# Performance work log

Measured on AMD Instinct MI355X. Metric: run time of the kernel, lower is better.

Reference implementation:

```python
import jax, jax.numpy as jnp
import numpy as np

VOCAB = 32000
EMB = 512
HEADS = 8
HEAD_DIM = EMB // HEADS
MLP = 2048
LAYERS = 6
KERNEL_EPS = 1e-3  # performer generalized-attention kernel_epsilon
LN_EPS = 1e-6


def sinusoidal_pos_emb(seq_len, dim):
    pos = np.arange(seq_len)[:, None].astype(np.float32)
    div = np.exp(np.arange(0, dim, 2).astype(np.float32) * (-np.log(10000.0) / dim))
    pe = np.zeros((seq_len, dim), dtype=np.float32)
    pe[:, 0::2] = np.sin(pos * div)
    pe[:, 1::2] = np.cos(pos * div)
    return jnp.asarray(pe)


def setup_inputs() -> dict:
    key = jax.random.key(0)
    ks = jax.random.split(key, 16)
    B, S = 4, 4096
    s_emb = 1.0 / np.sqrt(EMB)
    s_head = 1.0 / np.sqrt(HEAD_DIM)
    s_mlp = 1.0 / np.sqrt(MLP)
    return {
        'tokens': jax.random.randint(ks[0], (B, S), 0, VOCAB),
        'embed': jax.random.normal(ks[1], (VOCAB, EMB), jnp.float32) * s_emb,
        'Wq': jax.random.normal(ks[2], (LAYERS, EMB, HEADS, HEAD_DIM), jnp.float32) * s_emb,
        'Wk': jax.random.normal(ks[3], (LAYERS, EMB, HEADS, HEAD_DIM), jnp.float32) * s_emb,
        'Wv': jax.random.normal(ks[4], (LAYERS, EMB, HEADS, HEAD_DIM), jnp.float32) * s_emb,
        'Wo': jax.random.normal(ks[5], (LAYERS, HEADS, HEAD_DIM, EMB), jnp.float32) * s_head,
        'ln1_s': jnp.ones((LAYERS, EMB), jnp.float32),
        'ln1_b': jnp.zeros((LAYERS, EMB), jnp.float32),
        'W1': jax.random.normal(ks[6], (LAYERS, EMB, MLP), jnp.float32) * s_emb,
        'b1': jnp.zeros((LAYERS, MLP), jnp.float32),
        'W2': jax.random.normal(ks[7], (LAYERS, MLP, EMB), jnp.float32) * s_mlp,
        'b2': jnp.zeros((LAYERS, EMB), jnp.float32),
        'ln2_s': jnp.ones((LAYERS, EMB), jnp.float32),
        'ln2_b': jnp.zeros((LAYERS, EMB), jnp.float32),
        'lnf_s': jnp.ones((EMB,), jnp.float32),
        'lnf_b': jnp.zeros((EMB,), jnp.float32),
    }


def layer_norm(x, s, b):
    mu = jnp.mean(x, axis=-1, keepdims=True)
    var = jnp.mean(jnp.square(x - mu), axis=-1, keepdims=True)
    return (x - mu) * jax.lax.rsqrt(var + LN_EPS) * s + b


def favor_generalized_attention(x, Wq, Wk, Wv, Wo):
    # Performer generalized attention, deterministic ReLU feature map,
    # renormalized (bidirectional): O(S * m * d) linear attention.
    q = jnp.einsum('bsd,dhf->bshf', x, Wq)
    k = jnp.einsum('bsd,dhf->bshf', x, Wk)
    v = jnp.einsum('bsd,dhf->bshf', x, Wv)
    pq = jax.nn.relu(q) + KERNEL_EPS  # phi(q): [B,S,H,F]
    pk = jax.nn.relu(k) + KERNEL_EPS  # phi(k)
    kv = jnp.einsum('bshf,bshe->bhfe', pk, v)          # [B,H,F,E]
    num = jnp.einsum('bshf,bhfe->bshe', pq, kv)        # numerator
    den = jnp.einsum('bshf,bhf->bsh', pq, pk.sum(axis=1))  # renormalizer
    attn = num / den[..., None]
    return jnp.einsum('bshe,hed->bsd', attn, Wo)


def reference(tokens, embed, Wq, Wk, Wv, Wo, ln1_s, ln1_b, W1, b1, W2, b2,
              ln2_s, ln2_b, lnf_s, lnf_b):
    B, S = tokens.shape
    x = embed[tokens] + sinusoidal_pos_emb(S, EMB)[None, :, :]
    for l in range(LAYERS):
        h = layer_norm(x, ln1_s[l], ln1_b[l])
        x = x + favor_generalized_attention(h, Wq[l], Wk[l], Wv[l], Wo[l])
        h = layer_norm(x, ln2_s[l], ln2_b[l])
        h = jax.nn.gelu(h @ W1[l] + b1[l]) @ W2[l] + b2[l]
        x = x + h
    return layer_norm(x, lnf_s, lnf_b)
```

## Files before the change

### kernel.cpp

```cpp
#include <hip/hip_runtime.h>

typedef float f32x4 __attribute__((ext_vector_type(4)));
typedef __bf16 bf16x8 __attribute__((ext_vector_type(8)));

#define NROWS 16384
#define SEQ   4096
#define EMBD  512
#define MLPD  2048

__device__ inline float gelu_tanh(float x) {
    float t = 0.7978845608028654f * (x + 0.044715f * x * x * x);
    float e = __expf(2.f * t);
    float th = 1.f - 2.f / (1.f + e);
    return 0.5f * x * (1.f + th);
}

#define GLOAD16(gp, lp)                                                        \
    __builtin_amdgcn_global_load_lds(                                          \
        (const __attribute__((address_space(1))) void*)(gp),                   \
        (__attribute__((address_space(3))) void*)(lp), 16, 0, 0)

__global__ void pos_kernel(float* __restrict__ pos) {
    int i = blockIdx.x * 256 + threadIdx.x;
    int s = i >> 8, j = i & 255;
    float div = __expf((float)j * (-2.f * 9.210340371976184f / 512.f));
    float a = (float)s * div;
    pos[(size_t)s * 512 + 2 * j]     = sinf(a);
    pos[(size_t)s * 512 + 2 * j + 1] = cosf(a);
}

__global__ void embed_kernel(const int* __restrict__ tokens,
                             const float* __restrict__ embed,
                             const float* __restrict__ pos,
                             float* __restrict__ x) {
    int row = blockIdx.x;
    int t = threadIdx.x;
    int s = row & (SEQ - 1);
    int tok = tokens[row];
    f32x4 e = *(const f32x4*)(embed + (size_t)tok * 512 + t * 4);
    f32x4 p = *(const f32x4*)(pos + (size_t)s * 512 + t * 4);
    e += p;
    *(f32x4*)(x + (size_t)row * 512 + t * 4) = e;
}

__global__ void transpose_bf16(const float* __restrict__ in, __bf16* __restrict__ out,
                               int K, int N, size_t in_lstride, size_t out_lstride) {
    __shared__ float tile[32][33];
    in  += (size_t)blockIdx.z * in_lstride;
    out += (size_t)blockIdx.z * out_lstride;
    int n0 = blockIdx.x * 32, k0 = blockIdx.y * 32;
    int tx = threadIdx.x, ty = threadIdx.y;
    #pragma unroll
    for (int i = 0; i < 32; i += 8)
        tile[ty + i][tx] = in[(size_t)(k0 + ty + i) * N + n0 + tx];
    __syncthreads();
    #pragma unroll
    for (int i = 0; i < 32; i += 8)
        out[(size_t)(n0 + ty + i) * K + k0 + tx] = (__bf16)tile[tx][ty + i];
}

template<int OUTBF>
__global__ __launch_bounds__(256) void ln_kernel(
    const float* __restrict__ x, const float* __restrict__ gamma,
    const float* __restrict__ beta, __bf16* __restrict__ outb,
    float* __restrict__ outf) {
    int lane = threadIdx.x & 63;
    size_t row = (size_t)blockIdx.x * 4 + (threadIdx.x >> 6);
    const float* xr = x + row * 512 + lane * 8;
    f32x4 v0 = *(const f32x4*)xr;
    f32x4 v1 = *(const f32x4*)(xr + 4);
    float sum = (v0[0] + v0[1]) + (v0[2] + v0[3]) + (v1[0] + v1[1]) + (v1[2] + v1[3]);
    #pragma unroll
    for (int off = 32; off; off >>= 1) sum += __shfl_xor(sum, off);
    float mu = sum * (1.f / 512.f);
    float vs = 0.f;
    #pragma unroll
    for (int j = 0; j < 4; j++) {
        float d0 = v0[j] - mu; vs += d0 * d0;
        float d1 = v1[j] - mu; vs += d1 * d1;
    }
    #pragma unroll
    for (int off = 32; off; off >>= 1) vs += __shfl_xor(vs, off);
    float inv = rsqrtf(vs * (1.f / 512.f) + 1e-6f);
    const float* gp = gamma + lane * 8;
    const float* bp = beta + lane * 8;
    f32x4 g0 = *(const f32x4*)gp, g1 = *(const f32x4*)(gp + 4);
    f32x4 bb0 = *(const f32x4*)bp, bb1 = *(const f32x4*)(bp + 4);
    float o[8];
    #pragma unroll
    for (int j = 0; j < 4; j++) {
        o[j]     = (v0[j] - mu) * inv * g0[j] + bb0[j];
        o[4 + j] = (v1[j] - mu) * inv * g1[j] + bb1[j];
    }
    if (OUTBF) {
        bf16x8 ov;
        #pragma unroll
        for (int j = 0; j < 8; j++) ov[j] = (__bf16)o[j];
        *(bf16x8*)(outb + row * 512 + lane * 8) = ov;
    } else {
        f32x4 o0 = {o[0], o[1], o[2], o[3]};
        f32x4 o1 = {o[4], o[5], o[6], o[7]};
        *(f32x4*)(outf + row * 512 + lane * 8) = o0;
        *(f32x4*)(outf + row * 512 + lane * 8 + 4) = o1;
    }
}

template<int EPI, int K, int BM>
__global__ __launch_bounds__(256, 4) void gemm_bt(
    const __bf16* __restrict__ A, const __bf16* __restrict__ BT,
    float* __restrict__ Cf, __bf16* __restrict__ Cb,
    const float* __restrict__ bias, int N, int nbn) {
    constexpr int NT = K / 32;
    constexpr int AL = BM / 64;
    constexpr int NREP = (BM == 128) ? 4 : 2;
    __shared__ __align__(16) __bf16 Asm[3][BM * 32];
    __shared__ __align__(16) __bf16 Bsm[3][128 * 32];
    const int t = threadIdx.x;
    const int lane = t & 63;
    const int wave = t >> 6;
    const int wr = (BM == 128) ? (wave >> 1) : 0;
    const int wc = (BM == 128) ? (wave & 1) : wave;
    const int nblk = gridDim.x;
    const int q = nblk >> 3, r = nblk & 7;
    const int xcd = blockIdx.x & 7, loc = blockIdx.x >> 3;
    const int swz = (xcd < r ? xcd * (q + 1) : r * (q + 1) + (xcd - r) * q) + loc;
    const int m0 = (swz / nbn) * BM, n0 = (swz % nbn) * 128;
    const int fr = lane & 15, fc = lane >> 4;

    const __bf16* Aps[AL];
    const __bf16* Bps[2];
    int aslot[AL], bslot[2];
    #pragma unroll
    for (int j = 0; j < AL; j++) {
        int slot = t + 256 * j;
        int row = slot >> 2, cp = slot & 3;
        int sc = cp ^ ((row >> 1) & 3);
        Aps[j] = A + (size_t)(m0 + row) * K + sc * 8;
        aslot[j] = slot * 8;
    }
    #pragma unroll
    for (int j = 0; j < 2; j++) {
        int slot = t + 256 * j;
        int row = slot >> 2, cp = slot & 3;
        int sc = cp ^ ((row >> 1) & 3);
        Bps[j] = BT + (size_t)(n0 + row) * K + sc * 8;
        bslot[j] = slot * 8;
    }

    f32x4 acc[4][NREP];
    #pragma unroll
    for (int m = 0; m < 4; m++)
        #pragma unroll
        for (int n = 0; n < NREP; n++)
            acc[m][n] = (f32x4){0.f, 0.f, 0.f, 0.f};

    auto stage = [&](int koff, __bf16* Ad, __bf16* Bd) {
        #pragma unroll
        for (int j = 0; j < AL; j++) GLOAD16(Aps[j] + koff, Ad + aslot[j]);
        #pragma unroll
        for (int j = 0; j < 2; j++) GLOAD16(Bps[j] + koff, Bd + bslot[j]);
    };

    __bf16 *A0 = Asm[0], *A1 = Asm[1], *A2 = Asm[2];
    __bf16 *B0 = Bsm[0], *B1 = Bsm[1], *B2 = Bsm[2];
    stage(0, A0, B0);
    stage(32, A1, B1);

    for (int s = 0; s < NT; s++) {
        if (s + 2 < NT) {
            stage((s + 2) * 32, A2, B2);
            if constexpr (BM == 128) asm volatile("s_waitcnt vmcnt(8)" ::: "memory");
            else                     asm volatile("s_waitcnt vmcnt(6)" ::: "memory");
        } else if (s + 1 < NT) {
            if constexpr (BM == 128) asm volatile("s_waitcnt vmcnt(4)" ::: "memory");
            else                     asm volatile("s_waitcnt vmcnt(3)" ::: "memory");
        } else {
            asm volatile("s_waitcnt vmcnt(0)" ::: "memory");
        }
        __builtin_amdgcn_s_barrier();

        bf16x8 af[4], bfr[NREP];
        #pragma unroll
        for (int m = 0; m < 4; m++) {
            int ra = wr * 64 + m * 16 + fr;
            af[m] = *(const bf16x8*)(A0 + ra * 32 + ((fc ^ ((ra >> 1) & 3)) << 3));
        }
        #pragma unroll
        for (int n = 0; n < NREP; n++) {
            int rb = wc * (16 * NREP) + n * 16 + fr;
            bfr[n] = *(const bf16x8*)(B0 + rb * 32 + ((fc ^ ((rb >> 1) & 3)) << 3));
        }
        __builtin_amdgcn_s_setprio(1);
        #pragma unroll
        for (int m = 0; m < 4; m++)
            #pragma unroll
            for (int n = 0; n < NREP; n++)
                acc[m][n] = __builtin_amdgcn_mfma_f32_16x16x32_bf16(af[m], bfr[n], acc[m][n], 0, 0, 0);
        __builtin_amdgcn_s_setprio(0);
        __builtin_amdgcn_s_barrier();

        __bf16* ta = A0; A0 = A1; A1 = A2; A2 = ta;
        __bf16* tb = B0; B0 = B1; B1 = B2; B2 = tb;
    }

    const int cr = (lane >> 4) * 4;
    const int cc = lane & 15;
    #pragma unroll
    for (int m = 0; m < 4; m++) {
        #pragma unroll
        for (int n = 0; n < NREP; n++) {
            #pragma unroll
            for (int r2 = 0; r2 < 4; r2++) {
                int grow = m0 + wr * 64 + m * 16 + cr + r2;
                int gcol = n0 + wc * (16 * NREP) + n * 16 + cc;
                size_t idx = (size_t)grow * N + gcol;
                float val = acc[m][n][r2];
                if (EPI == 1) {
                    if (gcol < 1024) val = fmaxf(val, 0.f) + 1e-3f;
                    Cb[idx] = (__bf16)val;
                } else if (EPI == 2) {
                    Cf[idx] += val;
                } else if (EPI == 3) {
                    val += bias[gcol];
                    Cb[idx] = (__bf16)gelu_tanh(val);
                } else if (EPI == 4) {
                    Cf[idx] += val + bias[gcol];
                } else {
                    Cf[idx] = val;
                }
            }
        }
    }
}

__global__ __launch_bounds__(256) void kv_partial(const __bf16* __restrict__ qkvb,
                                                  float* __restrict__ part) {
    int bh = blockIdx.x;
    int chunk = blockIdx.y;
    int b = bh >> 3, hh = bh & 7;
    int t = threadIdx.x;
    int f = t & 63, eg = t >> 6;
    size_t base = ((size_t)b * SEQ + (size_t)chunk * 64) * 1536;
    const __bf16* kcol = qkvb + base + 512 + hh * 64 + f;
    const __bf16* vrow = qkvb + base + 1024 + hh * 64 + eg * 16;
    float psum = 0.f;
    f32x4 a0 = {0.f,0.f,0.f,0.f}, a1 = a0, a2 = a0, a3 = a0;
    for (int s = 0; s < 64; s++) {
        size_t o = (size_t)s * 1536;
        float pk = (float)kcol[o];
        psum += pk;
        bf16x8 w0 = *(const bf16x8*)(vrow + o);
        bf16x8 w1 = *(const bf16x8*)(vrow + o + 8);
        #pragma unroll
        for (int j = 0; j < 4; j++) {
            a0[j] += (float)w0[j]     * pk;
            a1[j] += (float)w0[4 + j] * pk;
            a2[j] += (float)w1[j]     * pk;
            a3[j] += (float)w1[4 + j] * pk;
        }
    }
    float* dst = part + ((size_t)chunk * 32 + bh) * 4160 + (size_t)f * 65 + eg * 16;
    #pragma unroll
    for (int j = 0; j < 4; j++) { dst[j] = a0[j]; dst[4+j] = a1[j]; dst[8+j] = a2[j]; dst[12+j] = a3[j]; }
    if (eg == 0) dst[64] = psum;
}

__global__ void kv_reduce(const float* __restrict__ part, float* __restrict__ kvfin) {
    int i = blockIdx.x * 256 + threadIdx.x;
    if (i >= 32 * 4160) return;
    float s = 0.f;
    #pragma unroll 8
    for (int c = 0; c < 64; c++) s += part[(size_t)c * (32 * 4160) + i];
    kvfin[i] = s;
}

__global__ __launch_bounds__(256) void num_attn(const __bf16* __restrict__ qkvb,
                                                const float* __restrict__ kvfin,
                                                __bf16* __restrict__ attn) {
    __shared__ float kvs[64][68];
    __shared__ float ps[64];
    int bh = blockIdx.x, chunk = blockIdx.y;
    int b = bh >> 3, hh = bh & 7;
    const float* src = kvfin + (size_t)bh * 4160;
    for (int i = threadIdx.x; i < 4160; i += 256) {
        int f = i / 65, e = i - f * 65;
        if (e < 64) kvs[f][e] = src[i]; else ps[f] = src[i];
    }
    __syncthreads();
    int t = threadIdx.x;
    int r = t >> 1, e0 = (t & 1) * 32;
    size_t row = (size_t)b * SEQ + (size_t)chunk * 128 + r;
    const __bf16* pqr = qkvb + row * 1536 + hh * 64;
    float pq[64];
    #pragma unroll
    for (int j = 0; j < 8; j++) {
        bf16x8 v = *(const bf16x8*)(pqr + 8 * j);
        #pragma unroll
        for (int k = 0; k < 8; k++) pq[8 * j + k] = (float)v[k];
    }
    float den = 0.f;
    #pragma unroll
    for (int f = 0; f < 64; f++) den += pq[f] * ps[f];
    f32x4 acc[8];
    #pragma unroll
    for (int j = 0; j < 8; j++) acc[j] = (f32x4){0.f,0.f,0.f,0.f};
    for (int f = 0; f < 64; f++) {
        float p = pq[f];
        #pragma unroll
        for (int j = 0; j < 8; j++) acc[j] += *(const f32x4*)(&kvs[f][e0 + 4 * j]) * p;
    }
    float rd = 1.f / den;
    __bf16* op = attn + row * 512 + hh * 64 + e0;
    #pragma unroll
    for (int j2 = 0; j2 < 4; j2++) {
        bf16x8 ov;
        #pragma unroll
        for (int k = 0; k < 8; k++) ov[k] = (__bf16)(acc[j2 * 2 + k / 4][k % 4] * rd);
        *(bf16x8*)(op + j2 * 8) = ov;
    }
}

extern "C" void kernel_launch(void* const* d_in, const int* in_sizes, int n_in,
                              void* d_out, int out_size, void* d_ws, size_t ws_size,
                              hipStream_t stream) {
    const int*   tokens = (const int*)d_in[0];
    const float* embed  = (const float*)d_in[1];
    const float* Wq     = (const float*)d_in[2];
    const float* Wk     = (const float*)d_in[3];
    const float* Wv     = (const float*)d_in[4];
    const float* Wo     = (const float*)d_in[5];
    const float* ln1_s  = (const float*)d_in[6];
    const float* ln1_b  = (const float*)d_in[7];
    const float* W1     = (const float*)d_in[8];
    const float* b1     = (const float*)d_in[9];
    const float* W2     = (const float*)d_in[10];
    const float* b2     = (const float*)d_in[11];
    const float* ln2_s  = (const float*)d_in[12];
    const float* ln2_b  = (const float*)d_in[13];
    const float* lnf_s  = (const float*)d_in[14];
    const float* lnf_b  = (const float*)d_in[15];
    float* out = (float*)d_out;

    float* ws = (float*)d_ws;
    size_t off = 0;
    float* pos = ws;               off += 2097152;
    float* x   = ws + off;         off += 8388608;
    __bf16* h    = (__bf16*)(ws + off); off += 4194304;
    __bf16* attn = (__bf16*)(ws + off); off += 4194304;
    __bf16* qkvb = (__bf16*)(ws + off);
    __bf16* hid  = (__bf16*)(ws + off); off += 16777216;
    float* kvpart = ws + off;      off += 64 * 32 * 4160;
    float* kvfin  = ws + off;      off += 32 * 4160;
    __bf16* wbuf  = (__bf16*)(ws + off);

    pos_kernel<<<4096, 256, 0, stream>>>(pos);
    transpose_bf16<<<dim3(16, 16, 6), dim3(32, 8), 0, stream>>>(Wq, wbuf,          512, 512,  262144, 3145728);
    transpose_bf16<<<dim3(16, 16, 6), dim3(32, 8), 0, stream>>>(Wk, wbuf + 262144, 512, 512,  262144, 3145728);
    transpose_bf16<<<dim3(16, 16, 6), dim3(32, 8), 0, stream>>>(Wv, wbuf + 524288, 512, 512,  262144, 3145728);
    transpose_bf16<<<dim3(16, 16, 6), dim3(32, 8), 0, stream>>>(Wo, wbuf + 786432, 512, 512,  262144, 3145728);
    transpose_bf16<<<dim3(64, 16, 6), dim3(32, 8), 0, stream>>>(W1, wbuf + 1048576, 512, 2048, 1048576, 3145728);
    transpose_bf16<<<dim3(16, 64, 6), dim3(32, 8), 0, stream>>>(W2, wbuf + 2097152, 2048, 512, 1048576, 3145728);
    embed_kernel<<<16384, 128, 0, stream>>>(tokens, embed, pos, x);

    for (int l = 0; l < 6; l++) {
        const __bf16* wl = wbuf + (size_t)l * 3145728;
        ln_kernel<1><<<4096, 256, 0, stream>>>(x, ln1_s + l * 512, ln1_b + l * 512, h, nullptr);
        gemm_bt<1, 512, 128><<<1536, 256, 0, stream>>>(h, wl, nullptr, qkvb, nullptr, 1536, 12);
        kv_partial<<<dim3(32, 64), 256, 0, stream>>>(qkvb, kvpart);
        kv_reduce<<<520, 256, 0, stream>>>(kvpart, kvfin);
        num_attn<<<dim3(32, 32), 256, 0, stream>>>(qkvb, kvfin, attn);
        gemm_bt<2, 512, 64><<<1024, 256, 0, stream>>>(attn, wl + 786432, x, nullptr, nullptr, 512, 4);
        ln_kernel<1><<<4096, 256, 0, stream>>>(x, ln2_s + l * 512, ln2_b + l * 512, h, nullptr);
        gemm_bt<3, 512, 128><<<2048, 256, 0, stream>>>(h, wl + 1048576, nullptr, hid, b1 + (size_t)l * 2048, 2048, 16);
        gemm_bt<4, 2048, 64><<<1024, 256, 0, stream>>>(hid, wl + 2097152, x, nullptr, b2 + (size_t)l * 512, 512, 4);
    }
    ln_kernel<0><<<4096, 256, 0, stream>>>(x, lnf_s, lnf_b, nullptr, out);
}
```

Baseline: 1.761 ms.

## Use MFMA for performer numerator and nontemporal stores in GEMM epilogues

Rewrites the num_attn kernel to compute phi(q)·KV with bf16 MFMA 16x16x32 instructions instead of scalar FMA loops, staging the KV matrix in shared memory as bf16. The denominator is computed separately per row with a shuffle reduction. GEMM epilogues also switch to nontemporal stores to reduce cache pollution. The change trades precision in KV (now bf16) for matrix-core throughput, and the bf16 output is now written with scattered 2-byte stores.

Result: slower. 1.978 ms (+12.3%).

```diff
diff --git a/kernel.cpp b/kernel.cpp
--- a/kernel.cpp
+++ b/kernel.cpp
@@ -13,6 +13,10 @@
     float e = __expf(2.f * t);
     float th = 1.f - 2.f / (1.f + e);
     return 0.5f * x * (1.f + th);
+}
+
+__device__ inline void nt_store_bf16(__bf16 v, __bf16* p) {
+    __builtin_nontemporal_store(__builtin_bit_cast(unsigned short, v), (unsigned short*)p);
 }
 
 #define GLOAD16(gp, lp)                                                        \
@@ -217,14 +221,14 @@
                 float val = acc[m][n][r2];
                 if (EPI == 1) {
                     if (gcol < 1024) val = fmaxf(val, 0.f) + 1e-3f;
-                    Cb[idx] = (__bf16)val;
+                    nt_store_bf16((__bf16)val, &Cb[idx]);
                 } else if (EPI == 2) {
-                    Cf[idx] += val;
+                    __builtin_nontemporal_store(Cf[idx] + val, &Cf[idx]);
                 } else if (EPI == 3) {
                     val += bias[gcol];
-                    Cb[idx] = (__bf16)gelu_tanh(val);
+                    nt_store_bf16((__bf16)gelu_tanh(val), &Cb[idx]);
                 } else if (EPI == 4) {
-                    Cf[idx] += val + bias[gcol];
+                    __builtin_nontemporal_store(Cf[idx] + val + bias[gcol], &Cf[idx]);
                 } else {
                     Cf[idx] = val;
                 }
@@ -277,46 +281,78 @@
 __global__ __launch_bounds__(256) void num_attn(const __bf16* __restrict__ qkvb,
                                                 const float* __restrict__ kvfin,
                                                 __bf16* __restrict__ attn) {
-    __shared__ float kvs[64][68];
+    __shared__ __bf16 kvb[64][68];
     __shared__ float ps[64];
+    __shared__ float dens[128];
     int bh = blockIdx.x, chunk = blockIdx.y;
     int b = bh >> 3, hh = bh & 7;
     const float* src = kvfin + (size_t)bh * 4160;
-    for (int i = threadIdx.x; i < 4160; i += 256) {
-        int f = i / 65, e = i - f * 65;
-        if (e < 64) kvs[f][e] = src[i]; else ps[f] = src[i];
-    }
+    int t = threadIdx.x;
+    for (int i = t; i < 4096; i += 256) {
+        int f = i >> 6, e = i & 63;
+        kvb[f][e] = (__bf16)src[f * 65 + e];
+    }
+    if (t < 64) ps[t] = src[t * 65 + 64];
     __syncthreads();
-    int t = threadIdx.x;
-    int r = t >> 1, e0 = (t & 1) * 32;
-    size_t row = (size_t)b * SEQ + (size_t)chunk * 128 + r;
-    const __bf16* pqr = qkvb + row * 1536 + hh * 64;
-    float pq[64];
-    #pragma unroll
-    for (int j = 0; j < 8; j++) {
-        bf16x8 v = *(const bf16x8*)(pqr + 8 * j);
-        #pragma unroll
-        for (int k = 0; k < 8; k++) pq[8 * j + k] = (float)v[k];
-    }
-    float den = 0.f;
-    #pragma unroll
-    for (int f = 0; f < 64; f++) den += pq[f] * ps[f];
-    f32x4 acc[8];
-    #pragma unroll
-    for (int j = 0; j < 8; j++) acc[j] = (f32x4){0.f,0.f,0.f,0.f};
-    for (int f = 0; f < 64; f++) {
-        float p = pq[f];
-        #pragma unroll
-        for (int j = 0; j < 8; j++) acc[j] += *(const f32x4*)(&kvs[f][e0 + 4 * j]) * p;
-    }
-    float rd = 1.f / den;
-    __bf16* op = attn + row * 512 + hh * 64 + e0;
-    #pragma unroll
-    for (int j2 = 0; j2 < 4; j2++) {
-        bf16x8 ov;
-        #pragma unroll
-        for (int k = 0; k < 8; k++) ov[k] = (__bf16)(acc[j2 * 2 + k / 4][k % 4] * rd);
-        *(bf16x8*)(op + j2 * 8) = ov;
+    {
+        int rr = t >> 1, hf = t & 1;
+        size_t grow = (size_t)b * SEQ + (size_t)chunk * 128 + rr;
+        const __bf16* pqr = qkvb + grow * 1536 + hh * 64 + hf * 32;
+        float d = 0.f;
+        #pragma unroll
+        for (int j = 0; j < 4; j++) {
+            bf16x8 v = *(const bf16x8*)(pqr + 8 * j);
+            #pragma unroll
+            for (int k = 0; k < 8; k++) d += (float)v[k] * ps[hf * 32 + 8 * j + k];
+        }
+        d += __shfl_xor(d, 1);
+        if (hf == 0) dens[rr] = d;
+    }
+    const int lane = t & 63, w = t >> 6;
+    const int fr = lane & 15, fc = lane >> 4;
+    size_t rowbase = (size_t)b * SEQ + (size_t)chunk * 128 + w * 32;
+    bf16x8 a[2][2];
+    #pragma unroll
+    for (int rt = 0; rt < 2; rt++)
+        #pragma unroll
+        for (int ks = 0; ks < 2; ks++)
+            a[rt][ks] = *(const bf16x8*)(qkvb + (rowbase + rt * 16 + fr) * 1536 + hh * 64 + ks * 32 + fc * 8);
+    __syncthreads();
+    bf16x8 bfrag[4][2];
+    #pragma unroll
+    for (int n = 0; n < 4; n++)
+        #pragma unroll
+        for (int ks = 0; ks < 2; ks++) {
+            bf16x8 bv;
+            #pragma unroll
+            for (int j = 0; j < 8; j++) bv[j] = kvb[ks * 32 + fc * 8 + j][n * 16 + fr];
+            bfrag[n][ks] = bv;
+        }
+    f32x4 acc[2][4];
+    #pragma unroll
+    for (int rt = 0; rt < 2; rt++)
+        #pragma unroll
+        for (int n = 0; n < 4; n++)
+            acc[rt][n] = (f32x4){0.f, 0.f, 0.f, 0.f};
+    #pragma unroll
+    for (int ks = 0; ks < 2; ks++)
+        #pragma unroll
+        for (int rt = 0; rt < 2; rt++)
+            #pragma unroll
+            for (int n = 0; n < 4; n++)
+                acc[rt][n] = __builtin_amdgcn_mfma_f32_16x16x32_bf16(a[rt][ks], bfrag[n][ks], acc[rt][n], 0, 0, 0);
+    const int cr = (lane >> 4) * 4, cc = lane & 15;
+    #pragma unroll
+    for (int rt = 0; rt < 2; rt++) {
+        #pragma unroll
+        for (int r2 = 0; r2 < 4; r2++) {
+            int lr = w * 32 + rt * 16 + cr + r2;
+            float rd = 1.f / dens[lr];
+            size_t grow = (size_t)b * SEQ + (size_t)chunk * 128 + lr;
+            #pragma unroll
+            for (int n = 0; n < 4; n++)
+                attn[grow * 512 + hh * 64 + n * 16 + cc] = (__bf16)(acc[rt][n][r2] * rd);
+        }
     }
 }
 
```
